# Kernel optimization log

Hardware: AMD Instinct MI355X
Metric: run time of the kernel (lower is better)

The kernel has to match this reference:

```python
import jax, jax.numpy as jnp
import numpy as np

N = 100_000   # nodes
E = 1_600_000 # edges
G, H1, H2, Z = 64, 64, 64, 32


def _w(k, o, i):
    return jax.random.normal(k, (o, i), jnp.float32) * (1.0 / np.sqrt(i))


def setup_inputs() -> dict:
    key = jax.random.key(0)
    ks = jax.random.split(key, 16)
    inp = {
        "x": jax.random.normal(ks[0], (N, G), jnp.float32),
        "edge_src": jax.random.randint(ks[1], (E,), 0, N, jnp.int32),
        "edge_dst": jax.random.randint(ks[2], (E,), 0, N, jnp.int32),
        "eps": jax.random.normal(ks[3], (N, Z), jnp.float32),
        "W1": _w(ks[4], H1, G),  "b1": jnp.zeros((H1,), jnp.float32),
        "W2": _w(ks[5], H2, H1), "b2": jnp.zeros((H2,), jnp.float32),
        "W31": _w(ks[6], Z, H2), "b31": jnp.zeros((Z,), jnp.float32),
        "W32": _w(ks[7], Z, H2), "b32": jnp.zeros((Z,), jnp.float32),
        "W4": _w(ks[8], H2, Z),  "b4": jnp.zeros((H2,), jnp.float32),
        "W5": _w(ks[9], H1, H2), "b5": jnp.zeros((H1,), jnp.float32),
        "W6": _w(ks[10], G, H1), "b6": jnp.zeros((G,), jnp.float32),
    }
    return inp


def _gcn(h, W, b, act, src, dst, norm):
    # message: h_src * norm_src, gathered per edge  [E, d]
    m = (h * norm)[src]
    # reduce: sum over incoming edges, scaled by norm_dst  [N, d]
    agg = jax.ops.segment_sum(m, dst, num_segments=N) * norm
    # node apply: linear + activation
    return act(agg @ W.T + b)


def reference(x, edge_src, edge_dst, eps,
              W1, b1, W2, b2, W31, b31, W32, b32, W4, b4, W5, b5, W6, b6):
    # symmetric GCN norm: deg^{-1/2} from in-degree
    deg = jax.ops.segment_sum(jnp.ones((E,), jnp.float32), edge_dst, num_segments=N)
    norm = jax.lax.rsqrt(jnp.maximum(deg, 1.0))[:, None]  # [N,1]

    relu = jax.nn.relu
    ident = lambda h: h

    h = _gcn(x, W1, b1, relu, edge_src, edge_dst, norm)
    h = _gcn(h, W2, b2, relu, edge_src, edge_dst, norm)
    mu = _gcn(h, W31, b31, ident, edge_src, edge_dst, norm)
    log_var = _gcn(h, W32, b32, ident, edge_src, edge_dst, norm)

    z = eps * jnp.exp(0.5 * log_var) + mu

    h = _gcn(z, W4, b4, relu, edge_src, edge_dst, norm)
    h = _gcn(h, W5, b5, relu, edge_src, edge_dst, norm)
    recon = _gcn(h, W6, b6, jax.nn.sigmoid, edge_src, edge_dst, norm)
    return recon, mu, log_var
```

## Files before the change

kernel.cpp:

```cpp
#include <hip/hip_runtime.h>
#include <hip/hip_fp16.h>
#include <math.h>

#define NN 100000
#define NE 1600000
#define NBKT 391
#define CHUNK 8192
#define NB1 ((NE + CHUNK - 1) / CHUNK)

__global__ __launch_bounds__(256) void p0_hist_kernel(const int* __restrict__ dst,
                                                      int* __restrict__ bcnt) {
    __shared__ int h[NBKT];
    for (int b = threadIdx.x; b < NBKT; b += 256) h[b] = 0;
    __syncthreads();
    int e0 = blockIdx.x * CHUNK;
    for (int k = 0; k < CHUNK / 256; ++k) {
        int e = e0 + threadIdx.x + k * 256;
        if (e < NE) atomicAdd(&h[dst[e] >> 8], 1);
    }
    __syncthreads();
    for (int b = threadIdx.x; b < NBKT; b += 256)
        if (h[b]) atomicAdd(&bcnt[b], h[b]);
}

__global__ void scan_buckets_kernel(const int* __restrict__ bcnt, int* __restrict__ bbase,
                                    int* __restrict__ bcur) {
    __shared__ int s[512];
    int tid = threadIdx.x;
    int v = (tid < NBKT) ? bcnt[tid] : 0;
    s[tid] = v;
    __syncthreads();
    for (int off = 1; off < 512; off <<= 1) {
        int t = (tid >= off) ? s[tid - off] : 0;
        __syncthreads();
        s[tid] += t;
        __syncthreads();
    }
    if (tid < NBKT) { int ex = s[tid] - v; bbase[tid] = ex; bcur[tid] = ex; }
    if (tid == NBKT) bbase[NBKT] = NE;
}

__global__ __launch_bounds__(256) void p1_scatter_kernel(const int* __restrict__ src,
                                                         const int* __restrict__ dst,
                                                         int* __restrict__ bcur,
                                                         int* __restrict__ gpair) {
    __shared__ int h[NBKT], rb[NBKT], hc[NBKT];
    int tid = threadIdx.x;
    for (int b = tid; b < NBKT; b += 256) { h[b] = 0; hc[b] = 0; }
    __syncthreads();
    int e0 = blockIdx.x * CHUNK;
    for (int k = 0; k < CHUNK / 256; ++k) {
        int e = e0 + tid + k * 256;
        if (e < NE) atomicAdd(&h[dst[e] >> 8], 1);
    }
    __syncthreads();
    for (int b = tid; b < NBKT; b += 256)
        rb[b] = h[b] ? atomicAdd(&bcur[b], h[b]) : 0;
    __syncthreads();
    for (int k = 0; k < CHUNK / 256; ++k) {
        int e = e0 + tid + k * 256;
        if (e < NE) {
            int d = dst[e], s = src[e];
            int b = d >> 8;
            int pos = rb[b] + atomicAdd(&hc[b], 1);
            gpair[pos] = (s << 8) | (d & 255);
        }
    }
}

__global__ __launch_bounds__(256) void p2_place_kernel(const int* __restrict__ gpair,
                                                       const int* __restrict__ bbase,
                                                       int* __restrict__ csr,
                                                       int* __restrict__ row_start,
                                                       float* __restrict__ nrm) {
    __shared__ int cnt[256], nexcl[256], pcnt[256];
    int b = blockIdx.x, tid = threadIdx.x;
    int s0 = bbase[b], s1 = bbase[b + 1];
    cnt[tid] = 0; pcnt[tid] = 0;
    __syncthreads();
    for (int i = s0 + tid; i < s1; i += 256)
        atomicAdd(&cnt[gpair[i] & 255], 1);
    __syncthreads();
    int v = cnt[tid];
    nexcl[tid] = v;
    __syncthreads();
    for (int off = 1; off < 256; off <<= 1) {
        int t = (tid >= off) ? nexcl[tid - off] : 0;
        __syncthreads();
        nexcl[tid] += t;
        __syncthreads();
    }
    int ex = nexcl[tid] - v;
    int node = (b << 8) + tid;
    if (node < NN) {
        row_start[node] = s0 + ex;
        nrm[node] = rsqrtf(fmaxf((float)v, 1.0f));
    }
    if (b == NBKT - 1 && tid == 0) row_start[NN] = NE;
    nexcl[tid] = s0 + ex;
    __syncthreads();
    for (int i = s0 + tid; i < s1; i += 256) {
        int p = gpair[i];
        int l = p & 255;
        int pos = nexcl[l] + atomicAdd(&pcnt[l], 1);
        csr[pos] = p >> 8;
    }
}

union H4 { uint2 u; __half2 h[2]; };

__global__ void scale_x_h_kernel(const float4* __restrict__ x4, const float* __restrict__ nrm,
                                 uint2* __restrict__ xs, int total4) {
    int i = blockIdx.x * blockDim.x + threadIdx.x;
    if (i < total4) {
        float nv = nrm[i >> 4];
        float4 v = x4[i];
        H4 w;
        w.h[0] = __floats2half2_rn(v.x * nv, v.y * nv);
        w.h[1] = __floats2half2_rn(v.z * nv, v.w * nv);
        xs[i] = w.u;
    }
}

template<int IN, int ACT, bool SCALE, bool DUAL>
__global__ __launch_bounds__(256) void gcn_fused_kernel(
        const __half* __restrict__ h,
        const float* __restrict__ nrm,
        const int* __restrict__ row_start,
        const int* __restrict__ csr,
        const float* __restrict__ Wa, const float* __restrict__ ba,
        const float* __restrict__ Wb, const float* __restrict__ bb,
        void* __restrict__ outv, float* __restrict__ out2,
        const float* __restrict__ eps, __half* __restrict__ zbuf) {
    constexpr int MLP = 8;
    __shared__ float Wt[64 * 65];
    __shared__ float bs[64];
    __shared__ __align__(16) float aggS[4][MLP][IN];

    int tid = threadIdx.x;
    if (DUAL) {
        for (int i = tid; i < 32 * 64; i += 256) {
            int o = i >> 6, k = i & 63;
            Wt[k * 65 + o]      = Wa[i];
            Wt[k * 65 + o + 32] = Wb[i];
        }
        if (tid < 32) { bs[tid] = ba[tid]; bs[tid + 32] = bb[tid]; }
    } else {
        for (int i = tid; i < 64 * IN; i += 256) {
            int o = i / IN, k = i % IN;
            Wt[k * 65 + o] = Wa[i];
        }
        if (tid < 64) bs[tid] = ba[tid];
    }
    __syncthreads();

    constexpr int RL  = IN / 4;
    constexpr int EPI = 64 / RL;
    int wave = tid >> 6, lane = tid & 63;
    int row_slot = lane / RL;
    int f4 = lane % RL;
    int nodeBase = (blockIdx.x * 4 + wave) * MLP;

    const uint2* hp = (const uint2*)h;

    int rsb[MLP], re[MLP];
#pragma unroll
    for (int i = 0; i < MLP; ++i) {
        rsb[i] = row_start[nodeBase + i];
        re[i]  = row_start[nodeBase + i + 1];
    }
    int maxd = 0;
#pragma unroll
    for (int i = 0; i < MLP; ++i) maxd = max(maxd, re[i] - rsb[i]);
#pragma unroll
    for (int i = 0; i < MLP; ++i) rsb[i] += row_slot;

    float4 acc[MLP];
#pragma unroll
    for (int i = 0; i < MLP; ++i) acc[i] = make_float4(0.f, 0.f, 0.f, 0.f);

    for (int t = 0; t < maxd; t += EPI) {
        int s[MLP]; float m[MLP];
#pragma unroll
        for (int i = 0; i < MLP; ++i) {
            int jj = rsb[i] + t;
            bool ok = jj < re[i];
            s[i] = csr[ok ? jj : 0];
            m[i] = ok ? 1.f : 0.f;
        }
        H4 v[MLP];
#pragma unroll
        for (int i = 0; i < MLP; ++i)
            v[i].u = hp[(size_t)s[i] * RL + f4];
#pragma unroll
        for (int i = 0; i < MLP; ++i) {
            float2 f01 = __half22float2(v[i].h[0]);
            float2 f23 = __half22float2(v[i].h[1]);
            acc[i].x = fmaf(m[i], f01.x, acc[i].x);
            acc[i].y = fmaf(m[i], f01.y, acc[i].y);
            acc[i].z = fmaf(m[i], f23.x, acc[i].z);
            acc[i].w = fmaf(m[i], f23.y, acc[i].w);
        }
    }

#pragma unroll
    for (int i = 0; i < MLP; ++i) {
        for (int o = RL; o < 64; o <<= 1) {
            acc[i].x += __shfl_xor(acc[i].x, o);
            acc[i].y += __shfl_xor(acc[i].y, o);
            acc[i].z += __shfl_xor(acc[i].z, o);
            acc[i].w += __shfl_xor(acc[i].w, o);
        }
    }

    if (row_slot == 0) {
#pragma unroll
        for (int i = 0; i < MLP; ++i)
            ((float4*)aggS[wave][i])[f4] = acc[i];
    }

#pragma unroll
    for (int i = 0; i < MLP; ++i) {
        int node = nodeBase + i;
        float oa = 0.f;
#pragma unroll
        for (int k = 0; k < IN; ++k)
            oa = fmaf(aggS[wave][i][k], Wt[k * 65 + lane], oa);
        float nv = nrm[node];
        oa = oa * nv + bs[lane];
        if (ACT == 1) oa = fmaxf(oa, 0.f);
        if (ACT == 2) oa = 1.f / (1.f + expf(-oa));

        if (DUAL) {
            float* mu_p = (float*)outv;
            if (lane < 32) mu_p[(size_t)node * 32 + lane]        = oa;
            else           out2[(size_t)node * 32 + (lane - 32)] = oa;
            float lv_v = __shfl(oa, (lane + 32) & 63);
            if (lane < 32) {
                float e = eps[(size_t)node * 32 + lane];
                zbuf[(size_t)node * 32 + lane] = __float2half((e * expf(0.5f * lv_v) + oa) * nv);
            }
        } else if (SCALE) {
            ((__half*)outv)[(size_t)node * 64 + lane] = __float2half(oa * nv);
        } else {
            ((float*)outv)[(size_t)node * 64 + lane] = oa;
        }
    }
}

extern "C" void kernel_launch(void* const* d_in, const int* in_sizes, int n_in,
                              void* d_out, int out_size, void* d_ws, size_t ws_size,
                              hipStream_t stream) {
    const float* x    = (const float*)d_in[0];
    const int*   esrc = (const int*)d_in[1];
    const int*   edst = (const int*)d_in[2];
    const float* eps  = (const float*)d_in[3];
    const float* W1  = (const float*)d_in[4];  const float* b1  = (const float*)d_in[5];
    const float* W2  = (const float*)d_in[6];  const float* b2  = (const float*)d_in[7];
    const float* W31 = (const float*)d_in[8];  const float* b31 = (const float*)d_in[9];
    const float* W32 = (const float*)d_in[10]; const float* b32 = (const float*)d_in[11];
    const float* W4  = (const float*)d_in[12]; const float* b4  = (const float*)d_in[13];
    const float* W5  = (const float*)d_in[14]; const float* b5  = (const float*)d_in[15];
    const float* W6  = (const float*)d_in[16]; const float* b6  = (const float*)d_in[17];

    float* outp  = (float*)d_out;
    float* recon = outp;
    float* mu    = outp + (size_t)NN * 64;
    float* lv    = mu   + (size_t)NN * 32;

    int* wsI       = (int*)d_ws;
    int* bcnt      = wsI;
    int* bbase     = bcnt + 392;
    int* bcur      = bbase + 392;
    int* row_start = bcur + 392;
    int* csr       = row_start + NN + 4;
    float* nrm     = (float*)(csr + NE);
    __half* hA     = (__half*)(nrm + NN);
    __half* hB     = hA + (size_t)NN * 64;
    int* gpair     = (int*)hA;

    const int SB = 256;
    const int fgrid = NN / 32;

    hipMemsetAsync(bcnt, 0, 392 * sizeof(int), stream);
    p0_hist_kernel<<<NB1, 256, 0, stream>>>(edst, bcnt);
    scan_buckets_kernel<<<1, 512, 0, stream>>>(bcnt, bbase, bcur);
    p1_scatter_kernel<<<NB1, 256, 0, stream>>>(esrc, edst, bcur, gpair);
    p2_place_kernel<<<NBKT, 256, 0, stream>>>(gpair, bbase, csr, row_start, nrm);

    scale_x_h_kernel<<<(NN * 16 + SB - 1) / SB, SB, 0, stream>>>((const float4*)x, nrm, (uint2*)hA, NN * 16);

    gcn_fused_kernel<64, 1, true,  false><<<fgrid, 256, 0, stream>>>(hA, nrm, row_start, csr, W1,  b1,  nullptr, nullptr, hB,    nullptr, nullptr, nullptr);
    gcn_fused_kernel<64, 1, true,  false><<<fgrid, 256, 0, stream>>>(hB, nrm, row_start, csr, W2,  b2,  nullptr, nullptr, hA,    nullptr, nullptr, nullptr);
    gcn_fused_kernel<64, 0, false, true ><<<fgrid, 256, 0, stream>>>(hA, nrm, row_start, csr, W31, b31, W32,     b32,     mu,    lv,      eps,     hB);
    gcn_fused_kernel<32, 1, true,  false><<<fgrid, 256, 0, stream>>>(hB, nrm, row_start, csr, W4,  b4,  nullptr, nullptr, hA,    nullptr, nullptr, nullptr);
    gcn_fused_kernel<64, 1, true,  false><<<fgrid, 256, 0, stream>>>(hA, nrm, row_start, csr, W5,  b5,  nullptr, nullptr, hB,    nullptr, nullptr, nullptr);
    gcn_fused_kernel<64, 2, false, false><<<fgrid, 256, 0, stream>>>(hB, nrm, row_start, csr, W6,  b6,  nullptr, nullptr, recon, nullptr, nullptr, nullptr);
}
```

Measured before the change: 620.5 us.

## Split GCN aggregation into two source-range passes for gather locality

Each node's CSR neighbor list is now partitioned by source index (below or above half the node count). A new pre-pass kernel aggregates the low-half sources and stores partial sums in fp16, and the fused kernel then aggregates the high half, adds the partial and applies the linear layer. The aim is to shrink the gathered feature working set per pass so it fits in cache better. In exchange it adds an extra launch per layer, writes and reads a partial buffer, and rounds the partial sums to fp16.

New measurement: 979.0 us. 1.58x slower.

```diff
diff --git a/kernel.cpp b/kernel.cpp
--- a/kernel.cpp
+++ b/kernel.cpp
@@ -7,6 +7,7 @@
 #define NBKT 391
 #define CHUNK 8192
 #define NB1 ((NE + CHUNK - 1) / CHUNK)
+#define HALFN 50000
 
 __global__ __launch_bounds__(256) void p0_hist_kernel(const int* __restrict__ dst,
                                                       int* __restrict__ bcnt) {
@@ -72,14 +73,19 @@
                                                        const int* __restrict__ bbase,
                                                        int* __restrict__ csr,
                                                        int* __restrict__ row_start,
+                                                       int* __restrict__ row_mid,
                                                        float* __restrict__ nrm) {
-    __shared__ int cnt[256], nexcl[256], pcnt[256];
+    __shared__ int cnt[256], cntLo[256], nexcl[256], baseL[256], baseH[256], pl[256], ph[256];
     int b = blockIdx.x, tid = threadIdx.x;
     int s0 = bbase[b], s1 = bbase[b + 1];
-    cnt[tid] = 0; pcnt[tid] = 0;
-    __syncthreads();
-    for (int i = s0 + tid; i < s1; i += 256)
-        atomicAdd(&cnt[gpair[i] & 255], 1);
+    cnt[tid] = 0; cntLo[tid] = 0; pl[tid] = 0; ph[tid] = 0;
+    __syncthreads();
+    for (int i = s0 + tid; i < s1; i += 256) {
+        int p = gpair[i];
+        int l = p & 255;
+        atomicAdd(&cnt[l], 1);
+        if ((p >> 8) < HALFN) atomicAdd(&cntLo[l], 1);
+    }
     __syncthreads();
     int v = cnt[tid];
     nexcl[tid] = v;
@@ -91,19 +97,24 @@
         __syncthreads();
     }
     int ex = nexcl[tid] - v;
+    int base = s0 + ex;
     int node = (b << 8) + tid;
     if (node < NN) {
-        row_start[node] = s0 + ex;
+        row_start[node] = base;
+        row_mid[node]   = base + cntLo[tid];
         nrm[node] = rsqrtf(fmaxf((float)v, 1.0f));
     }
     if (b == NBKT - 1 && tid == 0) row_start[NN] = NE;
-    nexcl[tid] = s0 + ex;
+    baseL[tid] = base;
+    baseH[tid] = base + cntLo[tid];
     __syncthreads();
     for (int i = s0 + tid; i < s1; i += 256) {
         int p = gpair[i];
         int l = p & 255;
-        int pos = nexcl[l] + atomicAdd(&pcnt[l], 1);
-        csr[pos] = p >> 8;
+        int s = p >> 8;
+        int pos = (s < HALFN) ? (baseL[l] + atomicAdd(&pl[l], 1))
+                              : (baseH[l] + atomicAdd(&ph[l], 1));
+        csr[pos] = s;
     }
 }
 
@@ -122,16 +133,94 @@
     }
 }
 
+template<int IN>
+__global__ __launch_bounds__(256) void gcn_part0_kernel(
+        const __half* __restrict__ h,
+        const int* __restrict__ rs_arr, const int* __restrict__ re_arr,
+        const int* __restrict__ csr,
+        uint2* __restrict__ pAgg) {
+    constexpr int MLP = 8;
+    constexpr int RL  = IN / 4;
+    constexpr int EPI = 64 / RL;
+    int tid = threadIdx.x;
+    int wave = tid >> 6, lane = tid & 63;
+    int row_slot = lane / RL;
+    int f4 = lane % RL;
+    int nodeBase = (blockIdx.x * 4 + wave) * MLP;
+    const uint2* hp = (const uint2*)h;
+
+    int rsb[MLP], re[MLP];
+#pragma unroll
+    for (int i = 0; i < MLP; ++i) {
+        rsb[i] = rs_arr[nodeBase + i];
+        re[i]  = re_arr[nodeBase + i];
+    }
+    int maxd = 0;
+#pragma unroll
+    for (int i = 0; i < MLP; ++i) maxd = max(maxd, re[i] - rsb[i]);
+#pragma unroll
+    for (int i = 0; i < MLP; ++i) rsb[i] += row_slot;
+
+    float4 acc[MLP];
+#pragma unroll
+    for (int i = 0; i < MLP; ++i) acc[i] = make_float4(0.f, 0.f, 0.f, 0.f);
+
+    for (int t = 0; t < maxd; t += EPI) {
+        int s[MLP]; float m[MLP];
+#pragma unroll
+        for (int i = 0; i < MLP; ++i) {
+            int jj = rsb[i] + t;
+            bool ok = jj < re[i];
+            s[i] = csr[ok ? jj : 0];
+            m[i] = ok ? 1.f : 0.f;
+        }
+        H4 v[MLP];
+#pragma unroll
+        for (int i = 0; i < MLP; ++i)
+            v[i].u = hp[(size_t)s[i] * RL + f4];
+#pragma unroll
+        for (int i = 0; i < MLP; ++i) {
+            float2 f01 = __half22float2(v[i].h[0]);
+            float2 f23 = __half22float2(v[i].h[1]);
+            acc[i].x = fmaf(m[i], f01.x, acc[i].x);
+            acc[i].y = fmaf(m[i], f01.y, acc[i].y);
+            acc[i].z = fmaf(m[i], f23.x, acc[i].z);
+            acc[i].w = fmaf(m[i], f23.y, acc[i].w);
+        }
+    }
+
+#pragma unroll
+    for (int i = 0; i < MLP; ++i) {
+        for (int o = RL; o < 64; o <<= 1) {
+            acc[i].x += __shfl_xor(acc[i].x, o);
+            acc[i].y += __shfl_xor(acc[i].y, o);
+            acc[i].z += __shfl_xor(acc[i].z, o);
+            acc[i].w += __shfl_xor(acc[i].w, o);
+        }
+    }
+
+    if (row_slot == 0) {
+#pragma unroll
+        for (int i = 0; i < MLP; ++i) {
+            H4 w;
+            w.h[0] = __floats2half2_rn(acc[i].x, acc[i].y);
+            w.h[1] = __floats2half2_rn(acc[i].z, acc[i].w);
+            pAgg[(size_t)(nodeBase + i) * RL + f4] = w.u;
+        }
+    }
+}
+
 template<int IN, int ACT, bool SCALE, bool DUAL>
 __global__ __launch_bounds__(256) void gcn_fused_kernel(
         const __half* __restrict__ h,
         const float* __restrict__ nrm,
-        const int* __restrict__ row_start,
+        const int* __restrict__ rs_arr, const int* __restrict__ re_arr,
         const int* __restrict__ csr,
         const float* __restrict__ Wa, const float* __restrict__ ba,
         const float* __restrict__ Wb, const float* __restrict__ bb,
         void* __restrict__ outv, float* __restrict__ out2,
-        const float* __restrict__ eps, __half* __restrict__ zbuf) {
+        const float* __restrict__ eps, __half* __restrict__ zbuf,
+        const uint2* __restrict__ pAgg) {
     constexpr int MLP = 8;
     __shared__ float Wt[64 * 65];
     __shared__ float bs[64];
@@ -166,8 +255,8 @@
     int rsb[MLP], re[MLP];
 #pragma unroll
     for (int i = 0; i < MLP; ++i) {
-        rsb[i] = row_start[nodeBase + i];
-        re[i]  = row_start[nodeBase + i + 1];
+        rsb[i] = rs_arr[nodeBase + i];
+        re[i]  = re_arr[nodeBase + i];
     }
     int maxd = 0;
 #pragma unroll
@@ -203,6 +292,13 @@
         }
     }
 
+    uint2 pv[MLP];
+    if (row_slot == 0) {
+#pragma unroll
+        for (int i = 0; i < MLP; ++i)
+            pv[i] = pAgg[(size_t)(nodeBase + i) * RL + f4];
+    }
+
 #pragma unroll
     for (int i = 0; i < MLP; ++i) {
         for (int o = RL; o < 64; o <<= 1) {
@@ -215,8 +311,14 @@
 
     if (row_slot == 0) {
 #pragma unroll
-        for (int i = 0; i < MLP; ++i)
+        for (int i = 0; i < MLP; ++i) {
+            H4 w; w.u = pv[i];
+            float2 a01 = __half22float2(w.h[0]);
+            float2 a23 = __half22float2(w.h[1]);
+            acc[i].x += a01.x; acc[i].y += a01.y;
+            acc[i].z += a23.x; acc[i].w += a23.y;
             ((float4*)aggS[wave][i])[f4] = acc[i];
+        }
     }
 
 #pragma unroll
@@ -273,11 +375,13 @@
     int* bbase     = bcnt + 392;
     int* bcur      = bbase + 392;
     int* row_start = bcur + 392;
-    int* csr       = row_start + NN + 4;
+    int* row_mid   = row_start + NN + 4;
+    int* csr       = row_mid + NN + 4;
     float* nrm     = (float*)(csr + NE);
-    __half* hA     = (__half*)(nrm + NN);
+    __half* pAgg   = (__half*)(nrm + NN);
+    __half* hA     = pAgg + (size_t)NN * 64;
     __half* hB     = hA + (size_t)NN * 64;
-    int* gpair     = (int*)hA;
+    int* gpair     = (int*)pAgg;
 
     const int SB = 256;
     const int fgrid = NN / 32;
@@ -286,14 +390,28 @@
     p0_hist_kernel<<<NB1, 256, 0, stream>>>(edst, bcnt);
     scan_buckets_kernel<<<1, 512, 0, stream>>>(bcnt, bbase, bcur);
     p1_scatter_kernel<<<NB1, 256, 0, stream>>>(esrc, edst, bcur, gpair);
-    p2_place_kernel<<<NBKT, 256, 0, stream>>>(gpair, bbase, csr, row_start, nrm);
+    p2_place_kernel<<<NBKT, 256, 0, stream>>>(gpair, bbase, csr, row_start, row_mid, nrm);
 
     scale_x_h_kernel<<<(NN * 16 + SB - 1) / SB, SB, 0, stream>>>((const float4*)x, nrm, (uint2*)hA, NN * 16);
 
-    gcn_fused_kernel<64, 1, true,  false><<<fgrid, 256, 0, stream>>>(hA, nrm, row_start, csr, W1,  b1,  nullptr, nullptr, hB,    nullptr, nullptr, nullptr);
-    gcn_fused_kernel<64, 1, true,  false><<<fgrid, 256, 0, stream>>>(hB, nrm, row_start, csr, W2,  b2,  nullptr, nullptr, hA,    nullptr, nullptr, nullptr);
-    gcn_fused_kernel<64, 0, false, true ><<<fgrid, 256, 0, stream>>>(hA, nrm, row_start, csr, W31, b31, W32,     b32,     mu,    lv,      eps,     hB);
-    gcn_fused_kernel<32, 1, true,  false><<<fgrid, 256, 0, stream>>>(hB, nrm, row_start, csr, W4,  b4,  nullptr, nullptr, hA,    nullptr, nullptr, nullptr);
-    gcn_fused_kernel<64, 1, true,  false><<<fgrid, 256, 0, stream>>>(hA, nrm, row_start, csr, W5,  b5,  nullptr, nullptr, hB,    nullptr, nullptr, nullptr);
-    gcn_fused_kernel<64, 2, false, false><<<fgrid, 256, 0, stream>>>(hB, nrm, row_start, csr, W6,  b6,  nullptr, nullptr, recon, nullptr, nullptr, nullptr);
-}
+    const uint2* pA = (const uint2*)pAgg;
+    uint2*       pW = (uint2*)pAgg;
+
+    gcn_part0_kernel<64><<<fgrid, 256, 0, stream>>>(hA, row_start, row_mid, csr, pW);
+    gcn_fused_kernel<64, 1, true,  false><<<fgrid, 256, 0, stream>>>(hA, nrm, row_mid, row_start + 1, csr, W1,  b1,  nullptr, nullptr, hB,    nullptr, nullptr, nullptr, pA);
+
+    gcn_part0_kernel<64><<<fgrid, 256, 0, stream>>>(hB, row_start, row_mid, csr, pW);
+    gcn_fused_kernel<64, 1, true,  false><<<fgrid, 256, 0, stream>>>(hB, nrm, row_mid, row_start + 1, csr, W2,  b2,  nullptr, nullptr, hA,    nullptr, nullptr, nullptr, pA);
+
+    gcn_part0_kernel<64><<<fgrid, 256, 0, stream>>>(hA, row_start, row_mid, csr, pW);
+    gcn_fused_kernel<64, 0, false, true ><<<fgrid, 256, 0, stream>>>(hA, nrm, row_mid, row_start + 1, csr, W31, b31, W32,     b32,     mu,    lv,      eps,     hB, pA);
+
+    gcn_part0_kernel<32><<<fgrid, 256, 0, stream>>>(hB, row_start, row_mid, csr, pW);
+    gcn_fused_kernel<32, 1, true,  false><<<fgrid, 256, 0, stream>>>(hB, nrm, row_mid, row_start + 1, csr, W4,  b4,  nullptr, nullptr, hA,    nullptr, nullptr, nullptr, pA);
+
+    gcn_part0_kernel<64><<<fgrid, 256, 0, stream>>>(hA, row_start, row_mid, csr, pW);
+    gcn_fused_kernel<64, 1, true,  false><<<fgrid, 256, 0, stream>>>(hA, nrm, row_mid, row_start + 1, csr, W5,  b5,  nullptr, nullptr, hB,    nullptr, nullptr, nullptr, pA);
+
+    gcn_part0_kernel<64><<<fgrid, 256, 0, stream>>>(hB, row_start, row_mid, csr, pW);
+    gcn_fused_kernel<64, 2, false, false><<<fgrid, 256, 0, stream>>>(hB, nrm, row_mid, row_start + 1, csr, W6,  b6,  nullptr, nullptr, recon, nullptr, nullptr, nullptr, pA);
+}
```

## Split neighbor gather into two source-range passes with separate apply kernel

Applied to the files above, without the earlier changes.

Each CSR row is split by source node index into a low half and a high half, recorded in a new row_mid array. Each layer now runs two gather passes, each reading only half of the feature table, so the working set may fit better in cache. The partial sums go through an fp16 buffer and a separate kernel applies the dense layer. This adds extra kernel launches, a global round trip for the partial aggregates, and an extra fp16 rounding of the intermediate sums.

Result: slower. 727.4 us (+17.2%).

```diff
diff --git a/kernel.cpp b/kernel.cpp
--- a/kernel.cpp
+++ b/kernel.cpp
@@ -7,6 +7,7 @@
 #define NBKT 391
 #define CHUNK 8192
 #define NB1 ((NE + CHUNK - 1) / CHUNK)
+#define HALFN 50000
 
 __global__ __launch_bounds__(256) void p0_hist_kernel(const int* __restrict__ dst,
                                                       int* __restrict__ bcnt) {
@@ -72,14 +73,19 @@
                                                        const int* __restrict__ bbase,
                                                        int* __restrict__ csr,
                                                        int* __restrict__ row_start,
+                                                       int* __restrict__ row_mid,
                                                        float* __restrict__ nrm) {
-    __shared__ int cnt[256], nexcl[256], pcnt[256];
+    __shared__ int cnt[256], cntLo[256], nexcl[256], baseL[256], baseH[256], pl[256], ph[256];
     int b = blockIdx.x, tid = threadIdx.x;
     int s0 = bbase[b], s1 = bbase[b + 1];
-    cnt[tid] = 0; pcnt[tid] = 0;
-    __syncthreads();
-    for (int i = s0 + tid; i < s1; i += 256)
-        atomicAdd(&cnt[gpair[i] & 255], 1);
+    cnt[tid] = 0; cntLo[tid] = 0; pl[tid] = 0; ph[tid] = 0;
+    __syncthreads();
+    for (int i = s0 + tid; i < s1; i += 256) {
+        int p = gpair[i];
+        int l = p & 255;
+        atomicAdd(&cnt[l], 1);
+        if ((p >> 8) < HALFN) atomicAdd(&cntLo[l], 1);
+    }
     __syncthreads();
     int v = cnt[tid];
     nexcl[tid] = v;
@@ -91,19 +97,24 @@
         __syncthreads();
     }
     int ex = nexcl[tid] - v;
+    int base = s0 + ex;
     int node = (b << 8) + tid;
     if (node < NN) {
-        row_start[node] = s0 + ex;
+        row_start[node] = base;
+        row_mid[node]   = base + cntLo[tid];
         nrm[node] = rsqrtf(fmaxf((float)v, 1.0f));
     }
     if (b == NBKT - 1 && tid == 0) row_start[NN] = NE;
-    nexcl[tid] = s0 + ex;
+    baseL[tid] = base;
+    baseH[tid] = base + cntLo[tid];
     __syncthreads();
     for (int i = s0 + tid; i < s1; i += 256) {
         int p = gpair[i];
         int l = p & 255;
-        int pos = nexcl[l] + atomicAdd(&pcnt[l], 1);
-        csr[pos] = p >> 8;
+        int s = p >> 8;
+        int pos = (s < HALFN) ? (baseL[l] + atomicAdd(&pl[l], 1))
+                              : (baseH[l] + atomicAdd(&ph[l], 1));
+        csr[pos] = s;
     }
 }
 
@@ -122,12 +133,101 @@
     }
 }
 
+template<int IN, bool ACC>
+__global__ __launch_bounds__(256) void gcn_gather_kernel(
+        const __half* __restrict__ h,
+        const int* __restrict__ rs_arr, const int* __restrict__ re_arr,
+        const int* __restrict__ csr,
+        uint2* __restrict__ pAgg) {
+    constexpr int MLP = 8;
+    constexpr int RL  = IN / 4;
+    constexpr int EPI = 64 / RL;
+    int tid = threadIdx.x;
+    int wave = tid >> 6, lane = tid & 63;
+    int row_slot = lane / RL;
+    int f4 = lane % RL;
+    int nodeBase = (blockIdx.x * 4 + wave) * MLP;
+    const uint2* hp = (const uint2*)h;
+
+    int rsb[MLP], re[MLP];
+#pragma unroll
+    for (int i = 0; i < MLP; ++i) {
+        rsb[i] = rs_arr[nodeBase + i];
+        re[i]  = re_arr[nodeBase + i];
+    }
+    int maxd = 0;
+#pragma unroll
+    for (int i = 0; i < MLP; ++i) maxd = max(maxd, re[i] - rsb[i]);
+#pragma unroll
+    for (int i = 0; i < MLP; ++i) rsb[i] += row_slot;
+
+    float4 acc[MLP];
+#pragma unroll
+    for (int i = 0; i < MLP; ++i) acc[i] = make_float4(0.f, 0.f, 0.f, 0.f);
+
+    for (int t = 0; t < maxd; t += EPI) {
+        int s[MLP]; float m[MLP];
+#pragma unroll
+        for (int i = 0; i < MLP; ++i) {
+            int jj = rsb[i] + t;
+            bool ok = jj < re[i];
+            s[i] = csr[ok ? jj : 0];
+            m[i] = ok ? 1.f : 0.f;
+        }
+        H4 v[MLP];
+#pragma unroll
+        for (int i = 0; i < MLP; ++i)
+            v[i].u = hp[(size_t)s[i] * RL + f4];
+#pragma unroll
+        for (int i = 0; i < MLP; ++i) {
+            float2 f01 = __half22float2(v[i].h[0]);
+            float2 f23 = __half22float2(v[i].h[1]);
+            acc[i].x = fmaf(m[i], f01.x, acc[i].x);
+            acc[i].y = fmaf(m[i], f01.y, acc[i].y);
+            acc[i].z = fmaf(m[i], f23.x, acc[i].z);
+            acc[i].w = fmaf(m[i], f23.y, acc[i].w);
+        }
+    }
+
+#pragma unroll
+    for (int i = 0; i < MLP; ++i) {
+        for (int o = RL; o < 64; o <<= 1) {
+            acc[i].x += __shfl_xor(acc[i].x, o);
+            acc[i].y += __shfl_xor(acc[i].y, o);
+            acc[i].z += __shfl_xor(acc[i].z, o);
+            acc[i].w += __shfl_xor(acc[i].w, o);
+        }
+    }
+
+    if (row_slot == 0) {
+        if (ACC) {
+            uint2 old[MLP];
+#pragma unroll
+            for (int i = 0; i < MLP; ++i)
+                old[i] = pAgg[(size_t)(nodeBase + i) * RL + f4];
+#pragma unroll
+            for (int i = 0; i < MLP; ++i) {
+                H4 o4; o4.u = old[i];
+                float2 a01 = __half22float2(o4.h[0]);
+                float2 a23 = __half22float2(o4.h[1]);
+                acc[i].x += a01.x; acc[i].y += a01.y;
+                acc[i].z += a23.x; acc[i].w += a23.y;
+            }
+        }
+#pragma unroll
+        for (int i = 0; i < MLP; ++i) {
+            H4 w;
+            w.h[0] = __floats2half2_rn(acc[i].x, acc[i].y);
+            w.h[1] = __floats2half2_rn(acc[i].z, acc[i].w);
+            pAgg[(size_t)(nodeBase + i) * RL + f4] = w.u;
+        }
+    }
+}
+
 template<int IN, int ACT, bool SCALE, bool DUAL>
-__global__ __launch_bounds__(256) void gcn_fused_kernel(
-        const __half* __restrict__ h,
+__global__ __launch_bounds__(256) void gcn_apply_kernel(
+        const uint2* __restrict__ pAgg,
         const float* __restrict__ nrm,
-        const int* __restrict__ row_start,
-        const int* __restrict__ csr,
         const float* __restrict__ Wa, const float* __restrict__ ba,
         const float* __restrict__ Wb, const float* __restrict__ bb,
         void* __restrict__ outv, float* __restrict__ out2,
@@ -155,68 +255,19 @@
     __syncthreads();
 
     constexpr int RL  = IN / 4;
-    constexpr int EPI = 64 / RL;
+    constexpr int RPP = 64 / RL;
     int wave = tid >> 6, lane = tid & 63;
     int row_slot = lane / RL;
     int f4 = lane % RL;
     int nodeBase = (blockIdx.x * 4 + wave) * MLP;
 
-    const uint2* hp = (const uint2*)h;
-
-    int rsb[MLP], re[MLP];
-#pragma unroll
-    for (int i = 0; i < MLP; ++i) {
-        rsb[i] = row_start[nodeBase + i];
-        re[i]  = row_start[nodeBase + i + 1];
-    }
-    int maxd = 0;
-#pragma unroll
-    for (int i = 0; i < MLP; ++i) maxd = max(maxd, re[i] - rsb[i]);
-#pragma unroll
-    for (int i = 0; i < MLP; ++i) rsb[i] += row_slot;
-
-    float4 acc[MLP];
-#pragma unroll
-    for (int i = 0; i < MLP; ++i) acc[i] = make_float4(0.f, 0.f, 0.f, 0.f);
-
-    for (int t = 0; t < maxd; t += EPI) {
-        int s[MLP]; float m[MLP];
-#pragma unroll
-        for (int i = 0; i < MLP; ++i) {
-            int jj = rsb[i] + t;
-            bool ok = jj < re[i];
-            s[i] = csr[ok ? jj : 0];
-            m[i] = ok ? 1.f : 0.f;
-        }
-        H4 v[MLP];
-#pragma unroll
-        for (int i = 0; i < MLP; ++i)
-            v[i].u = hp[(size_t)s[i] * RL + f4];
-#pragma unroll
-        for (int i = 0; i < MLP; ++i) {
-            float2 f01 = __half22float2(v[i].h[0]);
-            float2 f23 = __half22float2(v[i].h[1]);
-            acc[i].x = fmaf(m[i], f01.x, acc[i].x);
-            acc[i].y = fmaf(m[i], f01.y, acc[i].y);
-            acc[i].z = fmaf(m[i], f23.x, acc[i].z);
-            acc[i].w = fmaf(m[i], f23.y, acc[i].w);
-        }
-    }
-
-#pragma unroll
-    for (int i = 0; i < MLP; ++i) {
-        for (int o = RL; o < 64; o <<= 1) {
-            acc[i].x += __shfl_xor(acc[i].x, o);
-            acc[i].y += __shfl_xor(acc[i].y, o);
-            acc[i].z += __shfl_xor(acc[i].z, o);
-            acc[i].w += __shfl_xor(acc[i].w, o);
-        }
-    }
-
-    if (row_slot == 0) {
-#pragma unroll
-        for (int i = 0; i < MLP; ++i)
-            ((float4*)aggS[wave][i])[f4] = acc[i];
+#pragma unroll
+    for (int p = 0; p < MLP / RPP; ++p) {
+        int r = p * RPP + row_slot;
+        H4 v; v.u = pAgg[(size_t)(nodeBase + r) * RL + f4];
+        float2 f01 = __half22float2(v.h[0]);
+        float2 f23 = __half22float2(v.h[1]);
+        ((float4*)aggS[wave][r])[f4] = make_float4(f01.x, f01.y, f23.x, f23.y);
     }
 
 #pragma unroll
@@ -273,11 +324,13 @@
     int* bbase     = bcnt + 392;
     int* bcur      = bbase + 392;
     int* row_start = bcur + 392;
-    int* csr       = row_start + NN + 4;
+    int* row_mid   = row_start + NN + 4;
+    int* csr       = row_mid + NN + 4;
     float* nrm     = (float*)(csr + NE);
-    __half* hA     = (__half*)(nrm + NN);
+    __half* pAgg   = (__half*)(nrm + NN);
+    __half* hA     = pAgg + (size_t)NN * 64;
     __half* hB     = hA + (size_t)NN * 64;
-    int* gpair     = (int*)hA;
+    int* gpair     = (int*)pAgg;
 
     const int SB = 256;
     const int fgrid = NN / 32;
@@ -286,14 +339,31 @@
     p0_hist_kernel<<<NB1, 256, 0, stream>>>(edst, bcnt);
     scan_buckets_kernel<<<1, 512, 0, stream>>>(bcnt, bbase, bcur);
     p1_scatter_kernel<<<NB1, 256, 0, stream>>>(esrc, edst, bcur, gpair);
-    p2_place_kernel<<<NBKT, 256, 0, stream>>>(gpair, bbase, csr, row_start, nrm);
+    p2_place_kernel<<<NBKT, 256, 0, stream>>>(gpair, bbase, csr, row_start, row_mid, nrm);
 
     scale_x_h_kernel<<<(NN * 16 + SB - 1) / SB, SB, 0, stream>>>((const float4*)x, nrm, (uint2*)hA, NN * 16);
 
-    gcn_fused_kernel<64, 1, true,  false><<<fgrid, 256, 0, stream>>>(hA, nrm, row_start, csr, W1,  b1,  nullptr, nullptr, hB,    nullptr, nullptr, nullptr);
-    gcn_fused_kernel<64, 1, true,  false><<<fgrid, 256, 0, stream>>>(hB, nrm, row_start, csr, W2,  b2,  nullptr, nullptr, hA,    nullptr, nullptr, nullptr);
-    gcn_fused_kernel<64, 0, false, true ><<<fgrid, 256, 0, stream>>>(hA, nrm, row_start, csr, W31, b31, W32,     b32,     mu,    lv,      eps,     hB);
-    gcn_fused_kernel<32, 1, true,  false><<<fgrid, 256, 0, stream>>>(hB, nrm, row_start, csr, W4,  b4,  nullptr, nullptr, hA,    nullptr, nullptr, nullptr);
-    gcn_fused_kernel<64, 1, true,  false><<<fgrid, 256, 0, stream>>>(hA, nrm, row_start, csr, W5,  b5,  nullptr, nullptr, hB,    nullptr, nullptr, nullptr);
-    gcn_fused_kernel<64, 2, false, false><<<fgrid, 256, 0, stream>>>(hB, nrm, row_start, csr, W6,  b6,  nullptr, nullptr, recon, nullptr, nullptr, nullptr);
-}
+    uint2* pW = (uint2*)pAgg;
+    const int* rm = row_mid;
+    const int* rsA = row_start;
+    const int* reA = row_start + 1;
+
+    gcn_gather_kernel<64, false><<<fgrid, 256, 0, stream>>>(hA, rsA, rm, csr, pW);
+    gcn_gather_kernel<64, true ><<<fgrid, 256, 0, stream>>>(hA, rm, reA, csr, pW);
+    gcn_apply_kernel<64, 1, true,  false><<<fgrid, 256, 0, stream>>>(pW, nrm, W1,  b1,  nullptr, nullptr, hB,    nullptr, nullptr, nullptr);
+    gcn_gather_kernel<64, false><<<fgrid, 256, 0, stream>>>(hB, rsA, rm, csr, pW);
+    gcn_gather_kernel<64, true ><<<fgrid, 256, 0, stream>>>(hB, rm, reA, csr, pW);
+    gcn_apply_kernel<64, 1, true,  false><<<fgrid, 256, 0, stream>>>(pW, nrm, W2,  b2,  nullptr, nullptr, hA,    nullptr, nullptr, nullptr);
+    gcn_gather_kernel<64, false><<<fgrid, 256, 0, stream>>>(hA, rsA, rm, csr, pW);
+    gcn_gather_kernel<64, true ><<<fgrid, 256, 0, stream>>>(hA, rm, reA, csr, pW);
+    gcn_apply_kernel<64, 0, false, true ><<<fgrid, 256, 0, stream>>>(pW, nrm, W31, b31, W32,     b32,     mu,    lv,      eps,     hB);
+    gcn_gather_kernel<32, false><<<fgrid, 256, 0, stream>>>(hB, rsA, rm, csr, pW);
+    gcn_gather_kernel<32, true ><<<fgrid, 256, 0, stream>>>(hB, rm, reA, csr, pW);
+    gcn_apply_kernel<32, 1, true,  false><<<fgrid, 256, 0, stream>>>(pW, nrm, W4,  b4,  nullptr, nullptr, hA,    nullptr, nullptr, nullptr);
+    gcn_gather_kernel<64, false><<<fgrid, 256, 0, stream>>>(hA, rsA, rm, csr, pW);
+    gcn_gather_kernel<64, true ><<<fgrid, 256, 0, stream>>>(hA, rm, reA, csr, pW);
+    gcn_apply_kernel<64, 1, true,  false><<<fgrid, 256, 0, stream>>>(pW, nrm, W5,  b5,  nullptr, nullptr, hB,    nullptr, nullptr, nullptr);
+    gcn_gather_kernel<64, false><<<fgrid, 256, 0, stream>>>(hB, rsA, rm, csr, pW);
+    gcn_gather_kernel<64, true ><<<fgrid, 256, 0, stream>>>(hB, rm, reA, csr, pW);
+    gcn_apply_kernel<64, 2, false, false><<<fgrid, 256, 0, stream>>>(pW, nrm, W6,  b6,  nullptr, nullptr, recon, nullptr, nullptr, nullptr);
+}
```
